# Optimization experiments

Hardware: AMD Instinct MI355X
Metric: run time of the kernel (lower is better)

## Reference

```python
import jax, jax.numpy as jnp
import numpy as np

G = 16  # self.group
K = 3   # unfold/fold kernel size


def setup_inputs() -> dict:
    key = jax.random.key(0)
    feature = jax.random.normal(key, (2, 128, 192, 192), dtype=jnp.float32)
    return {"feature": feature}


def reference(feature):
    B, C, H, W = feature.shape
    Cg = C // G
    Hm, Wm = H - K + 1, W - K + 1
    L = Hm * Wm

    # --- nn.Unfold(kernel_size=3), all groups at once ---
    # patches[b, c, k, y, x] with k = ki*3 + kj (channel-major flat = c*9 + k)
    slices = [feature[:, :, ki:ki + Hm, kj:kj + Wm] for ki in range(K) for kj in range(K)]
    patches = jnp.stack(slices, axis=2)                 # [B, C, 9, Hm, Wm]
    # per-group series flat dim is Cg*9 (order cg*9+k); chunk(9) -> reshape [9, Cg]
    motif = patches.reshape(B, G, Cg * 9, L).reshape(B, G, 9, Cg, L)  # [B,G,9,Cg,L]

    # --- cdist + diag=inf + argmin (squared distances: same argmin as p=2) ---
    gram = jnp.einsum('bgjcl,bgjdl->bgjcd', motif, motif)   # [B,G,9,Cg,Cg]
    sq = jnp.einsum('bgjcl,bgjcl->bgjc', motif, motif)      # [B,G,9,Cg]
    d2 = sq[..., :, None] + sq[..., None, :] - 2.0 * gram
    eye = jnp.eye(Cg, dtype=bool)
    d2 = jnp.where(eye, jnp.inf, d2)
    nn_idx = jnp.argmin(d2, axis=-1)                        # [B,G,9,Cg] int

    # --- torch.unique loop overwrites motif_new: only the LAST (max) unique
    # index and its count survive ---
    u_max = jnp.max(nn_idx, axis=-1)                        # [B,G,9]
    c_max = jnp.sum(nn_idx == u_max[..., None], axis=-1).astype(feature.dtype)  # [B,G,9]

    motif_nn = jnp.take_along_axis(motif, u_max[..., None, None], axis=3)  # [B,G,9,1,L]
    # float '//' in torch is floor division
    term = jnp.floor(motif * motif_nn * c_max[..., None, None] / Cg)
    # l == 0 branch drops the '+ motif' term
    batch_mask = (jnp.arange(B) != 0).astype(feature.dtype).reshape(B, 1, 1, 1, 1)
    out_ser = motif * batch_mask + term                     # [B,G,9,Cg,L]

    # --- nn.Fold: input layout reinterpreted as (channel, kernel) flat = c*9+k ---
    ser2 = out_ser.reshape(B, G, 9 * Cg, L).reshape(B, G, Cg, 9, Hm, Wm)
    out = jnp.zeros((B, G, Cg, H, W), feature.dtype)
    for k in range(K * K):
        ki, kj = k // K, k % K
        out = out.at[:, :, :, ki:ki + Hm, kj:kj + Wm].add(ser2[:, :, :, k])
    return out.reshape(B, C, H, W)
```

## Files before the change

### kernel.cpp

```cpp
#include <hip/hip_runtime.h>
#include <hip/hip_bf16.h>
#include <math.h>

#define BB 2
#define CC 128
#define GG 16
#define CG 8
#define HH 192
#define WW 192
#define HM 190
#define WM 190
#define LL (HM * WM)
#define HWSZ (HH * WW)
#define NTRIPLE (BB * GG * 9)
#define SPLIT 6
#define ROWS_PER_SLICE 32

typedef float float4a __attribute__((ext_vector_type(4), aligned(4)));
typedef float float4v __attribute__((ext_vector_type(4)));

__device__ float g_part[NTRIPLE * SPLIT * 36];
__device__ int g_rel[BB * GG * 72];
__device__ float g_scl[BB * GG * 72];

constexpr bool row_used(int J, int ci, int ki) {
  for (int d = 0; d < 8; ++d) {
    const int f = 8 * J + d;
    if ((f / 9 - (8 * J) / 9) == ci && (f % 9) / 3 == ki) return true;
  }
  return false;
}

template <int J>
__device__ __forceinline__ void gram_slice(const float* __restrict__ pA,
                                           const float* __restrict__ pB,
                                           int y0, int rows, int tid,
                                           float acc[36]) {
  constexpr int CA = (8 * J) / 9;
  constexpr int CB = (8 * J + 7) / 9;
  constexpr int NCH = (CB > CA) ? 2 : 1;

  const int ngrp = rows * 47;
  for (int q = tid; q < ngrp; q += 128) {
    const int y = y0 + q / 47;
    const int x0 = (q % 47) * 4;
    const int ro = y * WW + x0;

    float w[NCH][3][8];
#pragma unroll
    for (int ci = 0; ci < NCH; ++ci) {
      const float* pc = ci ? pB : pA;
#pragma unroll
      for (int ki = 0; ki < 3; ++ki) {
        if (row_used(J, ci, ki)) {
          const float4v a = *(const float4v*)(pc + ro + ki * WW);
          const float4v bq = *(const float4v*)(pc + ro + ki * WW + 4);
          w[ci][ki][0] = a.x; w[ci][ki][1] = a.y;
          w[ci][ki][2] = a.z; w[ci][ki][3] = a.w;
          w[ci][ki][4] = bq.x; w[ci][ki][5] = bq.y;
          w[ci][ki][6] = bq.z; w[ci][ki][7] = bq.w;
        }
      }
    }
#pragma unroll
    for (int d = 0; d < 8; ++d) {
      constexpr_helper_sq:;
      const int f = 8 * J + d;
      const int ci = f / 9 - CA;
      const int k = f % 9;
      const int ki = k / 3, kj = k % 3;
      float s = 0.0f;
#pragma unroll
      for (int e = 0; e < 4; ++e) s += w[ci][ki][kj + e] * w[ci][ki][kj + e];
      acc[d] += s;
    }
    int p = 8;
#pragma unroll
    for (int c = 0; c < 8; ++c) {
      const int f1 = 8 * J + c;
      const int ci1 = f1 / 9 - CA;
      const int k1 = f1 % 9;
      const int ki1 = k1 / 3, kj1 = k1 % 3;
#pragma unroll
      for (int d = c + 1; d < 8; ++d) {
        const int f2 = 8 * J + d;
        const int ci2 = f2 / 9 - CA;
        const int k2 = f2 % 9;
        const int ki2 = k2 / 3, kj2 = k2 % 3;
        float s = 0.0f;
#pragma unroll
        for (int e = 0; e < 4; ++e)
          s += w[ci1][ki1][kj1 + e] * w[ci2][ki2][kj2 + e];
        acc[p++] += s;
      }
    }
  }

  const int ncl = rows * 2;
  for (int t = tid; t < ncl; t += 128) {
    const int y = y0 + t / 2;
    const int x = 188 + (t & 1);
    float v[8];
#pragma unroll
    for (int d = 0; d < 8; ++d) {
      const int f = 8 * J + d;
      const int ci = f / 9 - CA;
      const int k = f % 9;
      const int ki = k / 3, kj = k % 3;
      v[d] = (ci ? pB : pA)[(y + ki) * WW + x + kj];
    }
#pragma unroll
    for (int d = 0; d < 8; ++d) acc[d] += v[d] * v[d];
    int p = 8;
#pragma unroll
    for (int c = 0; c < 8; ++c)
#pragma unroll
      for (int d = c + 1; d < 8; ++d) acc[p++] += v[c] * v[d];
  }
}

__global__ __launch_bounds__(128, 2) void phase1a_kernel(
    const float* __restrict__ feat) {
  const int B = blockIdx.x;
  const int xcd = B & 7;
  const int slot = B >> 3;
  const int unit = xcd * 4 + slot / 54;
  const int r = slot % 54;
  const int j = r / 6;
  const int sl = r % 6;
  const int b = unit >> 4;
  const int g = unit & 15;

  const int cA = (8 * j) / 9;
  const int cB = (8 * j + 7) / 9;
  const float* pA = feat + (size_t)(b * CC + g * CG + cA) * HWSZ;
  const float* pB = feat + (size_t)(b * CC + g * CG + cB) * HWSZ;

  const int y0 = sl * ROWS_PER_SLICE;
  const int y1 = (y0 + ROWS_PER_SLICE < HM) ? y0 + ROWS_PER_SLICE : HM;
  const int rows = y1 - y0;
  const int tid = (int)threadIdx.x;

  float acc[36];
#pragma unroll
  for (int i = 0; i < 36; ++i) acc[i] = 0.0f;

  switch (j) {
    case 0: gram_slice<0>(pA, pB, y0, rows, tid, acc); break;
    case 1: gram_slice<1>(pA, pB, y0, rows, tid, acc); break;
    case 2: gram_slice<2>(pA, pB, y0, rows, tid, acc); break;
    case 3: gram_slice<3>(pA, pB, y0, rows, tid, acc); break;
    case 4: gram_slice<4>(pA, pB, y0, rows, tid, acc); break;
    case 5: gram_slice<5>(pA, pB, y0, rows, tid, acc); break;
    case 6: gram_slice<6>(pA, pB, y0, rows, tid, acc); break;
    case 7: gram_slice<7>(pA, pB, y0, rows, tid, acc); break;
    default: gram_slice<8>(pA, pB, y0, rows, tid, acc); break;
  }

  __shared__ float red[36 * 2];
  const int lane = tid & 63;
  const int wave = tid >> 6;
#pragma unroll
  for (int i = 0; i < 36; ++i) {
    float v = acc[i];
    for (int o = 32; o > 0; o >>= 1) v += __shfl_down(v, o, 64);
    if (lane == 0) red[i * 2 + wave] = v;
  }
  __syncthreads();
  if (tid < 36) {
    const int i = tid;
    const int tri = unit * 9 + j;
    g_part[(tri * SPLIT + sl) * 36 + i] = red[i * 2] + red[i * 2 + 1];
  }
}

__global__ __launch_bounds__(64) void phase1b_kernel() {
  const int tri = blockIdx.x * 64 + (int)threadIdx.x;
  if (tri >= NTRIPLE) return;
  const int b = tri / (GG * 9);
  const int rem = tri % (GG * 9);
  const int g = rem / 9;
  const int j = rem % 9;

  float tot[36];
#pragma unroll
  for (int i = 0; i < 36; ++i) tot[i] = 0.0f;
  for (int s = 0; s < SPLIT; ++s)
#pragma unroll
    for (int i = 0; i < 36; ++i) tot[i] += g_part[(tri * SPLIT + s) * 36 + i];

  float sq[8], gm[8][8];
#pragma unroll
  for (int i = 0; i < 8; ++i) sq[i] = tot[i];
  {
    int p = 8;
    for (int c = 0; c < 8; ++c)
      for (int d = c + 1; d < 8; ++d) {
        gm[c][d] = tot[p];
        gm[d][c] = tot[p];
        ++p;
      }
  }
  int nn[8];
  for (int c = 0; c < 8; ++c) {
    float best = INFINITY;
    int bi = 0;
    for (int d = 0; d < 8; ++d) {
      if (d == c) continue;
      const float d2 = sq[c] + sq[d] - 2.0f * gm[c][d];
      if (d2 < best) {
        best = d2;
        bi = d;
      }
    }
    nn[c] = bi;
  }
  int um = 0;
  for (int c = 0; c < 8; ++c) um = um > nn[c] ? um : nn[c];
  int cnt = 0;
  for (int c = 0; c < 8; ++c) cnt += (nn[c] == um) ? 1 : 0;

  const float sc = (float)cnt * 0.125f;
  const int fn = j * 8 + um;
  const int cn = fn / 9;
  const int kn = fn % 9;
  const int kin = kn / 3, kjn = kn % 3;
  for (int d = 0; d < 8; ++d) {
    const int f = j * 8 + d;
    const int cl = f / 9;
    const int k = f % 9;
    const int ki = k / 3, kj = k % 3;
    const int rel = (cn - cl) * HWSZ + (kin - ki) * WW + (kjn - kj);
    const int tix = (b * GG + g) * 72 + f;
    g_rel[tix] = rel;
    g_scl[tix] = sc;
  }
}

__global__ __launch_bounds__(256) void phase2_main_kernel(
    const float* __restrict__ feat, float* __restrict__ out) {
  const int B = blockIdx.x;
  const int xcd = B & 7;
  const int slot = B >> 3;
  const int unit = xcd * 4 + slot / 144;
  const int r = slot % 144;
  const int cl = r / 18;
  const int blk = r % 18;
  const int plane = unit * 8 + cl;

  const int tbase = unit * 72 + cl * 9;
  int rel[9];
  float scl[9];
#pragma unroll
  for (int k = 0; k < 9; ++k) {
    rel[k] = g_rel[tbase + k];
    scl[k] = g_scl[tbase + k];
  }

  const float* pb = feat + (size_t)plane * HWSZ;
  float* ob = out + (size_t)plane * HWSZ;
  const bool b1 = (unit >= GG);
  const int i0 = blk * 2048 + (int)threadIdx.x * 4;

#pragma unroll
  for (int gidx = 0; gidx < 2; ++gidx) {
    const int inner = i0 + gidx * 1024;
    const int h = inner / WW;
    const int w0 = inner % WW;
    if (h >= 2 && h < HM && w0 >= 4 && w0 < 188) {
      const float* p = pb + inner;
      const float4v v = *(const float4v*)p;
      float4v acc = {0.0f, 0.0f, 0.0f, 0.0f};
#pragma unroll
      for (int k = 0; k < 9; ++k) {
        const float4a n = *(const float4a*)(p + rel[k]);
        const float s = scl[k];
        acc.x += floorf(v.x * n.x * s);
        acc.y += floorf(v.y * n.y * s);
        acc.z += floorf(v.z * n.z * s);
        acc.w += floorf(v.w * n.w * s);
      }
      if (b1) {
        acc.x += 9.0f * v.x;
        acc.y += 9.0f * v.y;
        acc.z += 9.0f * v.z;
        acc.w += 9.0f * v.w;
      }
      *(float4v*)(ob + inner) = acc;
    }
  }
}

__global__ __launch_bounds__(256) void phase2_edge_kernel(
    const float* __restrict__ feat, float* __restrict__ out) {
  const int gid = blockIdx.x * 256 + (int)threadIdx.x;
  const int plane = gid / 2272;
  const int ei = gid % 2272;
  int h, w;
  if (ei < 768) {
    const int r = ei / WW;
    h = (r < 2) ? r : r + 188;
    w = ei % WW;
  } else {
    const int e2 = ei - 768;
    h = 2 + (e2 >> 3);
    const int w8 = e2 & 7;
    w = (w8 < 4) ? w8 : w8 + 184;
  }
  const int g = (plane % CC) >> 3;
  const int cl = (plane % CC) & 7;
  const int tbase = ((plane / CC) * GG + g) * 72 + cl * 9;

  int rel[9];
  float scl[9];
#pragma unroll
  for (int k = 0; k < 9; ++k) {
    rel[k] = g_rel[tbase + k];
    scl[k] = g_scl[tbase + k];
  }

  const int idx = plane * HWSZ + h * WW + w;
  const float* p = feat + idx;
  const float v = *p;
  float acc = 0.0f;
  int nv = 0;
#pragma unroll
  for (int k = 0; k < 9; ++k) {
    const int ki = k / 3, kj = k % 3;
    const int y = h - ki, x = w - kj;
    const bool valid = ((unsigned)y < (unsigned)HM) & ((unsigned)x < (unsigned)WM);
    const int o = valid ? rel[k] : 0;
    const float n = p[o];
    const float fl = floorf(v * n * scl[k]);
    acc += valid ? fl : 0.0f;
    nv += valid ? 1 : 0;
  }
  if (plane >= CC) acc += (float)nv * v;
  out[idx] = acc;
}

extern "C" void kernel_launch(void* const* d_in, const int* in_sizes, int n_in,
                              void* d_out, int out_size, void* d_ws,
                              size_t ws_size, hipStream_t stream) {
  const float* feat = (const float*)d_in[0];
  float* out = (float*)d_out;
  (void)d_ws;
  (void)ws_size;

  phase1a_kernel<<<NTRIPLE * SPLIT, 128, 0, stream>>>(feat);
  phase1b_kernel<<<(NTRIPLE + 63) / 64, 64, 0, stream>>>();

  phase2_main_kernel<<<BB * CC * 18, 256, 0, stream>>>(feat, out);
  phase2_edge_kernel<<<2272, 256, 0, stream>>>(feat, out);
}
```

Baseline: 131.7 us.

## Fuse partial-gram reduction into phase1 and edge handling into phase2 main kernel

The separate phase1b reduction kernel is removed. The last-arriving block for each triple, found with an atomic counter and threadfences, now sums the split partials, computes the nearest-neighbour index and scale, and resets the counter. The separate edge kernel is also folded into the main phase2 kernel as a scalar fallback branch for border pixels. This removes two kernel launches and their inter-kernel gaps, at the cost of atomics, fences and some divergence in the edge blocks.

```diff
diff --git a/kernel.cpp b/kernel.cpp
--- a/kernel.cpp
+++ b/kernel.cpp
@@ -1,5 +1,4 @@
 #include <hip/hip_runtime.h>
-#include <hip/hip_bf16.h>
 #include <math.h>
 
 #define BB 2
@@ -22,6 +21,7 @@
 __device__ float g_part[NTRIPLE * SPLIT * 36];
 __device__ int g_rel[BB * GG * 72];
 __device__ float g_scl[BB * GG * 72];
+__device__ int g_cnt[NTRIPLE];
 
 constexpr bool row_used(int J, int ci, int ki) {
   for (int d = 0; d < 8; ++d) {
@@ -64,7 +64,6 @@
     }
 #pragma unroll
     for (int d = 0; d < 8; ++d) {
-      constexpr_helper_sq:;
       const int f = 8 * J + d;
       const int ci = f / 9 - CA;
       const int k = f % 9;
@@ -119,7 +118,7 @@
   }
 }
 
-__global__ __launch_bounds__(128, 2) void phase1a_kernel(
+__global__ __launch_bounds__(128, 2) void phase1_kernel(
     const float* __restrict__ feat) {
   const int B = blockIdx.x;
   const int xcd = B & 7;
@@ -167,77 +166,84 @@
     if (lane == 0) red[i * 2 + wave] = v;
   }
   __syncthreads();
+  const int tri = unit * 9 + j;
   if (tid < 36) {
-    const int i = tid;
-    const int tri = unit * 9 + j;
-    g_part[(tri * SPLIT + sl) * 36 + i] = red[i * 2] + red[i * 2 + 1];
-  }
-}
-
-__global__ __launch_bounds__(64) void phase1b_kernel() {
-  const int tri = blockIdx.x * 64 + (int)threadIdx.x;
-  if (tri >= NTRIPLE) return;
-  const int b = tri / (GG * 9);
-  const int rem = tri % (GG * 9);
-  const int g = rem / 9;
-  const int j = rem % 9;
-
-  float tot[36];
-#pragma unroll
-  for (int i = 0; i < 36; ++i) tot[i] = 0.0f;
-  for (int s = 0; s < SPLIT; ++s)
-#pragma unroll
-    for (int i = 0; i < 36; ++i) tot[i] += g_part[(tri * SPLIT + s) * 36 + i];
-
-  float sq[8], gm[8][8];
-#pragma unroll
-  for (int i = 0; i < 8; ++i) sq[i] = tot[i];
-  {
-    int p = 8;
-    for (int c = 0; c < 8; ++c)
-      for (int d = c + 1; d < 8; ++d) {
-        gm[c][d] = tot[p];
-        gm[d][c] = tot[p];
-        ++p;
-      }
-  }
-  int nn[8];
-  for (int c = 0; c < 8; ++c) {
-    float best = INFINITY;
-    int bi = 0;
-    for (int d = 0; d < 8; ++d) {
-      if (d == c) continue;
-      const float d2 = sq[c] + sq[d] - 2.0f * gm[c][d];
-      if (d2 < best) {
-        best = d2;
-        bi = d;
-      }
-    }
-    nn[c] = bi;
-  }
-  int um = 0;
-  for (int c = 0; c < 8; ++c) um = um > nn[c] ? um : nn[c];
-  int cnt = 0;
-  for (int c = 0; c < 8; ++c) cnt += (nn[c] == um) ? 1 : 0;
-
-  const float sc = (float)cnt * 0.125f;
-  const int fn = j * 8 + um;
-  const int cn = fn / 9;
-  const int kn = fn % 9;
-  const int kin = kn / 3, kjn = kn % 3;
-  for (int d = 0; d < 8; ++d) {
-    const int f = j * 8 + d;
+    g_part[(tri * SPLIT + sl) * 36 + tid] = red[tid * 2] + red[tid * 2 + 1];
+  }
+
+  __threadfence();
+  __shared__ int s_last;
+  if (tid == 0) s_last = (atomicAdd(&g_cnt[tri], 1) == SPLIT - 1) ? 1 : 0;
+  __syncthreads();
+  if (!s_last) return;
+  __threadfence();
+
+  __shared__ float s_tot[36];
+  if (tid < 36) {
+    float t = 0.0f;
+    for (int s = 0; s < SPLIT; ++s)
+      t += g_part[(tri * SPLIT + s) * 36 + tid];
+    s_tot[tid] = t;
+  }
+  __syncthreads();
+
+  __shared__ int s_um;
+  __shared__ float s_sc;
+  if (tid == 0) {
+    float sq[8], gm[8][8];
+#pragma unroll
+    for (int i = 0; i < 8; ++i) sq[i] = s_tot[i];
+    {
+      int p = 8;
+      for (int c = 0; c < 8; ++c)
+        for (int d = c + 1; d < 8; ++d) {
+          gm[c][d] = s_tot[p];
+          gm[d][c] = s_tot[p];
+          ++p;
+        }
+    }
+    int nn[8];
+    for (int c = 0; c < 8; ++c) {
+      float best = INFINITY;
+      int bi = 0;
+      for (int d = 0; d < 8; ++d) {
+        if (d == c) continue;
+        const float d2 = sq[c] + sq[d] - 2.0f * gm[c][d];
+        if (d2 < best) {
+          best = d2;
+          bi = d;
+        }
+      }
+      nn[c] = bi;
+    }
+    int um = 0;
+    for (int c = 0; c < 8; ++c) um = um > nn[c] ? um : nn[c];
+    int cnt = 0;
+    for (int c = 0; c < 8; ++c) cnt += (nn[c] == um) ? 1 : 0;
+    s_um = um;
+    s_sc = (float)cnt * 0.125f;
+    g_cnt[tri] = 0;
+  }
+  __syncthreads();
+
+  if (tid < 8) {
+    const int um = s_um;
+    const int fn = j * 8 + um;
+    const int cn = fn / 9;
+    const int kn = fn % 9;
+    const int kin = kn / 3, kjn = kn % 3;
+    const int f = j * 8 + tid;
     const int cl = f / 9;
     const int k = f % 9;
     const int ki = k / 3, kj = k % 3;
     const int rel = (cn - cl) * HWSZ + (kin - ki) * WW + (kjn - kj);
-    const int tix = (b * GG + g) * 72 + f;
+    const int tix = unit * 72 + f;
     g_rel[tix] = rel;
-    g_scl[tix] = sc;
-  }
-}
-
-__global__ __launch_bounds__(256) void phase2_main_kernel(
+    g_scl[tix] = s_sc;
+  }
+}
+
+__global__ __launch_bounds__(256) void phase2_kernel(
     const float* __restrict__ feat, float* __restrict__ out) {
   const int B = blockIdx.x;
   const int xcd = B & 7;
@@ -287,56 +293,31 @@
         acc.w += 9.0f * v.w;
       }
       *(float4v*)(ob + inner) = acc;
-    }
-  }
-}
-
-__global__ __launch_bounds__(256) void phase2_edge_kernel(
-    const float* __restrict__ feat, float* __restrict__ out) {
-  const int gid = blockIdx.x * 256 + (int)threadIdx.x;
-  const int plane = gid / 2272;
-  const int ei = gid % 2272;
-  int h, w;
-  if (ei < 768) {
-    const int r = ei / WW;
-    h = (r < 2) ? r : r + 188;
-    w = ei % WW;
-  } else {
-    const int e2 = ei - 768;
-    h = 2 + (e2 >> 3);
-    const int w8 = e2 & 7;
-    w = (w8 < 4) ? w8 : w8 + 184;
-  }
-  const int g = (plane % CC) >> 3;
-  const int cl = (plane % CC) & 7;
-  const int tbase = ((plane / CC) * GG + g) * 72 + cl * 9;
-
-  int rel[9];
-  float scl[9];
-#pragma unroll
-  for (int k = 0; k < 9; ++k) {
-    rel[k] = g_rel[tbase + k];
-    scl[k] = g_scl[tbase + k];
-  }
-
-  const int idx = plane * HWSZ + h * WW + w;
-  const float* p = feat + idx;
-  const float v = *p;
-  float acc = 0.0f;
-  int nv = 0;
-#pragma unroll
-  for (int k = 0; k < 9; ++k) {
-    const int ki = k / 3, kj = k % 3;
-    const int y = h - ki, x = w - kj;
-    const bool valid = ((unsigned)y < (unsigned)HM) & ((unsigned)x < (unsigned)WM);
-    const int o = valid ? rel[k] : 0;
-    const float n = p[o];
-    const float fl = floorf(v * n * scl[k]);
-    acc += valid ? fl : 0.0f;
-    nv += valid ? 1 : 0;
-  }
-  if (plane >= CC) acc += (float)nv * v;
-  out[idx] = acc;
+    } else {
+#pragma unroll
+      for (int e = 0; e < 4; ++e) {
+        const int w = w0 + e;
+        const float* p = pb + inner + e;
+        const float v = *p;
+        float acc = 0.0f;
+        int nv = 0;
+#pragma unroll
+        for (int k = 0; k < 9; ++k) {
+          const int ki = k / 3, kj = k % 3;
+          const int y = h - ki, x = w - kj;
+          const bool valid =
+              ((unsigned)y < (unsigned)HM) & ((unsigned)x < (unsigned)WM);
+          const int o = valid ? rel[k] : 0;
+          const float n = p[o];
+          const float fl = floorf(v * n * scl[k]);
+          acc += valid ? fl : 0.0f;
+          nv += valid ? 1 : 0;
+        }
+        if (b1) acc += (float)nv * v;
+        ob[inner + e] = acc;
+      }
+    }
+  }
 }
 
 extern "C" void kernel_launch(void* const* d_in, const int* in_sizes, int n_in,
@@ -346,10 +327,10 @@
   float* out = (float*)d_out;
   (void)d_ws;
   (void)ws_size;
-
-  phase1a_kernel<<<NTRIPLE * SPLIT, 128, 0, stream>>>(feat);
-  phase1b_kernel<<<(NTRIPLE + 63) / 64, 64, 0, stream>>>();
-
-  phase2_main_kernel<<<BB * CC * 18, 256, 0, stream>>>(feat, out);
-  phase2_edge_kernel<<<2272, 256, 0, stream>>>(feat, out);
-}
+  (void)in_sizes;
+  (void)n_in;
+  (void)out_size;
+
+  phase1_kernel<<<NTRIPLE * SPLIT, 128, 0, stream>>>(feat);
+  phase2_kernel<<<BB * CC * 18, 256, 0, stream>>>(feat, out);
+}
```

Result: slower. 206.1 us (+56.4%).

## Fuse edge handling into main phase2 kernel and widen phase1 blocks

Applied to the files above, without the earlier changes.

Phase1 now runs 256 threads per block instead of 128, and its cross-wave reduction covers four waves. The two phase2 kernels become one: each block covers a quarter plane over nine iterations, and border pixels go through an inline scalar path instead of a separate edge kernel. This removes one kernel launch and adds parallelism in the Gram pass, at the cost of higher register pressure and some divergence in the border branches.

```diff
diff --git a/kernel.cpp b/kernel.cpp
--- a/kernel.cpp
+++ b/kernel.cpp
@@ -1,5 +1,4 @@
 #include <hip/hip_runtime.h>
-#include <hip/hip_bf16.h>
 #include <math.h>
 
 #define BB 2
@@ -10,7 +9,6 @@
 #define WW 192
 #define HM 190
 #define WM 190
-#define LL (HM * WM)
 #define HWSZ (HH * WW)
 #define NTRIPLE (BB * GG * 9)
 #define SPLIT 6
@@ -41,7 +39,7 @@
   constexpr int NCH = (CB > CA) ? 2 : 1;
 
   const int ngrp = rows * 47;
-  for (int q = tid; q < ngrp; q += 128) {
+  for (int q = tid; q < ngrp; q += 256) {
     const int y = y0 + q / 47;
     const int x0 = (q % 47) * 4;
     const int ro = y * WW + x0;
@@ -64,7 +62,6 @@
     }
 #pragma unroll
     for (int d = 0; d < 8; ++d) {
-      constexpr_helper_sq:;
       const int f = 8 * J + d;
       const int ci = f / 9 - CA;
       const int k = f % 9;
@@ -97,7 +94,7 @@
   }
 
   const int ncl = rows * 2;
-  for (int t = tid; t < ncl; t += 128) {
+  for (int t = tid; t < ncl; t += 256) {
     const int y = y0 + t / 2;
     const int x = 188 + (t & 1);
     float v[8];
@@ -119,7 +116,7 @@
   }
 }
 
-__global__ __launch_bounds__(128, 2) void phase1a_kernel(
+__global__ __launch_bounds__(256, 4) void phase1_kernel(
     const float* __restrict__ feat) {
   const int B = blockIdx.x;
   const int xcd = B & 7;
@@ -157,20 +154,21 @@
     default: gram_slice<8>(pA, pB, y0, rows, tid, acc); break;
   }
 
-  __shared__ float red[36 * 2];
+  __shared__ float red[36 * 4];
   const int lane = tid & 63;
   const int wave = tid >> 6;
 #pragma unroll
   for (int i = 0; i < 36; ++i) {
     float v = acc[i];
     for (int o = 32; o > 0; o >>= 1) v += __shfl_down(v, o, 64);
-    if (lane == 0) red[i * 2 + wave] = v;
+    if (lane == 0) red[i * 4 + wave] = v;
   }
   __syncthreads();
   if (tid < 36) {
-    const int i = tid;
     const int tri = unit * 9 + j;
-    g_part[(tri * SPLIT + sl) * 36 + i] = red[i * 2] + red[i * 2 + 1];
+    g_part[(tri * SPLIT + sl) * 36 + tid] =
+        ((red[tid * 4] + red[tid * 4 + 1]) + red[tid * 4 + 2]) +
+        red[tid * 4 + 3];
   }
 }
 
@@ -237,16 +235,17 @@
   }
 }
 
-__global__ __launch_bounds__(256) void phase2_main_kernel(
+__global__ __launch_bounds__(256) void phase2_kernel(
     const float* __restrict__ feat, float* __restrict__ out) {
   const int B = blockIdx.x;
   const int xcd = B & 7;
   const int slot = B >> 3;
-  const int unit = xcd * 4 + slot / 144;
-  const int r = slot % 144;
-  const int cl = r / 18;
-  const int blk = r % 18;
+  const int unit = xcd * 4 + slot / 32;
+  const int r = slot % 32;
+  const int cl = r / 4;
+  const int qblk = r % 4;
   const int plane = unit * 8 + cl;
+  const int tid = (int)threadIdx.x;
 
   const int tbase = unit * 72 + cl * 9;
   int rel[9];
@@ -260,10 +259,9 @@
   const float* pb = feat + (size_t)plane * HWSZ;
   float* ob = out + (size_t)plane * HWSZ;
   const bool b1 = (unit >= GG);
-  const int i0 = blk * 2048 + (int)threadIdx.x * 4;
-
-#pragma unroll
-  for (int gidx = 0; gidx < 2; ++gidx) {
+  const int i0 = qblk * 9216 + tid * 4;
+
+  for (int gidx = 0; gidx < 9; ++gidx) {
     const int inner = i0 + gidx * 1024;
     const int h = inner / WW;
     const int w0 = inner % WW;
@@ -287,56 +285,31 @@
         acc.w += 9.0f * v.w;
       }
       *(float4v*)(ob + inner) = acc;
-    }
-  }
-}
-
-__global__ __launch_bounds__(256) void phase2_edge_kernel(
-    const float* __restrict__ feat, float* __restrict__ out) {
-  const int gid = blockIdx.x * 256 + (int)threadIdx.x;
-  const int plane = gid / 2272;
-  const int ei = gid % 2272;
-  int h, w;
-  if (ei < 768) {
-    const int r = ei / WW;
-    h = (r < 2) ? r : r + 188;
-    w = ei % WW;
-  } else {
-    const int e2 = ei - 768;
-    h = 2 + (e2 >> 3);
-    const int w8 = e2 & 7;
-    w = (w8 < 4) ? w8 : w8 + 184;
-  }
-  const int g = (plane % CC) >> 3;
-  const int cl = (plane % CC) & 7;
-  const int tbase = ((plane / CC) * GG + g) * 72 + cl * 9;
-
-  int rel[9];
-  float scl[9];
-#pragma unroll
-  for (int k = 0; k < 9; ++k) {
-    rel[k] = g_rel[tbase + k];
-    scl[k] = g_scl[tbase + k];
-  }
-
-  const int idx = plane * HWSZ + h * WW + w;
-  const float* p = feat + idx;
-  const float v = *p;
-  float acc = 0.0f;
-  int nv = 0;
-#pragma unroll
-  for (int k = 0; k < 9; ++k) {
-    const int ki = k / 3, kj = k % 3;
-    const int y = h - ki, x = w - kj;
-    const bool valid = ((unsigned)y < (unsigned)HM) & ((unsigned)x < (unsigned)WM);
-    const int o = valid ? rel[k] : 0;
-    const float n = p[o];
-    const float fl = floorf(v * n * scl[k]);
-    acc += valid ? fl : 0.0f;
-    nv += valid ? 1 : 0;
-  }
-  if (plane >= CC) acc += (float)nv * v;
-  out[idx] = acc;
+    } else {
+#pragma unroll
+      for (int e = 0; e < 4; ++e) {
+        const int w = w0 + e;
+        const float* p = pb + inner + e;
+        const float v = *p;
+        float acc = 0.0f;
+        int nv = 0;
+#pragma unroll
+        for (int k = 0; k < 9; ++k) {
+          const int ki = k / 3, kj = k % 3;
+          const int y = h - ki, x = w - kj;
+          const bool valid =
+              ((unsigned)y < (unsigned)HM) & ((unsigned)x < (unsigned)WM);
+          const int o = valid ? rel[k] : 0;
+          const float n = p[o];
+          const float fl = floorf(v * n * scl[k]);
+          acc += valid ? fl : 0.0f;
+          nv += valid ? 1 : 0;
+        }
+        if (b1) acc += (float)nv * v;
+        ob[inner + e] = acc;
+      }
+    }
+  }
 }
 
 extern "C" void kernel_launch(void* const* d_in, const int* in_sizes, int n_in,
@@ -346,10 +319,11 @@
   float* out = (float*)d_out;
   (void)d_ws;
   (void)ws_size;
-
-  phase1a_kernel<<<NTRIPLE * SPLIT, 128, 0, stream>>>(feat);
+  (void)in_sizes;
+  (void)n_in;
+  (void)out_size;
+
+  phase1_kernel<<<NTRIPLE * SPLIT, 256, 0, stream>>>(feat);
   phase1b_kernel<<<(NTRIPLE + 63) / 64, 64, 0, stream>>>();
-
-  phase2_main_kernel<<<BB * CC * 18, 256, 0, stream>>>(feat, out);
-  phase2_edge_kernel<<<2272, 256, 0, stream>>>(feat, out);
-}
+  phase2_kernel<<<BB * CC * 4, 256, 0, stream>>>(feat, out);
+}
```

Result: slower. 149.3 us (+13.3%).

## Stage gram-slice input rows in shared memory and parallelize per-triple reduction

Applied to the files above, without the earlier changes.

The phase-1 Gram kernel now copies each region's one or two channel rows (plus a 2-row halo) into LDS with coalesced float4 loads. The windowed dot products then read from LDS instead of issuing overlapping global loads. The row split moves from 6 slices of 32 rows to 8 regions of 24 rows, blocks grow to 256 threads, and the finalize kernel uses one block per triple so 36 threads sum the partials in parallel. This costs about 40 KB of LDS per block, which may limit occupancy, plus extra halo-row loads.

```diff
diff --git a/kernel.cpp b/kernel.cpp
--- a/kernel.cpp
+++ b/kernel.cpp
@@ -1,5 +1,4 @@
 #include <hip/hip_runtime.h>
-#include <hip/hip_bf16.h>
 #include <math.h>
 
 #define BB 2
@@ -10,11 +9,10 @@
 #define WW 192
 #define HM 190
 #define WM 190
-#define LL (HM * WM)
 #define HWSZ (HH * WW)
 #define NTRIPLE (BB * GG * 9)
-#define SPLIT 6
-#define ROWS_PER_SLICE 32
+#define SPLIT 8
+#define RREG 24
 
 typedef float float4a __attribute__((ext_vector_type(4), aligned(4)));
 typedef float float4v __attribute__((ext_vector_type(4)));
@@ -32,29 +30,26 @@
 }
 
 template <int J>
-__device__ __forceinline__ void gram_slice(const float* __restrict__ pA,
-                                           const float* __restrict__ pB,
-                                           int y0, int rows, int tid,
-                                           float acc[36]) {
+__device__ __forceinline__ void gram_region(float* s_ch, int rows, int tid,
+                                            float acc[36]) {
   constexpr int CA = (8 * J) / 9;
   constexpr int CB = (8 * J + 7) / 9;
   constexpr int NCH = (CB > CA) ? 2 : 1;
 
   const int ngrp = rows * 47;
-  for (int q = tid; q < ngrp; q += 128) {
-    const int y = y0 + q / 47;
+  for (int q = tid; q < ngrp; q += 256) {
+    const int ly = q / 47;
     const int x0 = (q % 47) * 4;
-    const int ro = y * WW + x0;
 
     float w[NCH][3][8];
 #pragma unroll
     for (int ci = 0; ci < NCH; ++ci) {
-      const float* pc = ci ? pB : pA;
 #pragma unroll
       for (int ki = 0; ki < 3; ++ki) {
         if (row_used(J, ci, ki)) {
-          const float4v a = *(const float4v*)(pc + ro + ki * WW);
-          const float4v bq = *(const float4v*)(pc + ro + ki * WW + 4);
+          const float* rp = s_ch + (ci * 26 + ly + ki) * 192 + x0;
+          const float4v a = *(const float4v*)rp;
+          const float4v bq = *(const float4v*)(rp + 4);
           w[ci][ki][0] = a.x; w[ci][ki][1] = a.y;
           w[ci][ki][2] = a.z; w[ci][ki][3] = a.w;
           w[ci][ki][4] = bq.x; w[ci][ki][5] = bq.y;
@@ -64,7 +59,6 @@
     }
 #pragma unroll
     for (int d = 0; d < 8; ++d) {
-      constexpr_helper_sq:;
       const int f = 8 * J + d;
       const int ci = f / 9 - CA;
       const int k = f % 9;
@@ -97,8 +91,8 @@
   }
 
   const int ncl = rows * 2;
-  for (int t = tid; t < ncl; t += 128) {
-    const int y = y0 + t / 2;
+  for (int t = tid; t < ncl; t += 256) {
+    const int ly = t / 2;
     const int x = 188 + (t & 1);
     float v[8];
 #pragma unroll
@@ -107,7 +101,7 @@
       const int ci = f / 9 - CA;
       const int k = f % 9;
       const int ki = k / 3, kj = k % 3;
-      v[d] = (ci ? pB : pA)[(y + ki) * WW + x + kj];
+      v[d] = s_ch[(ci * 26 + ly + ki) * 192 + x + kj];
     }
 #pragma unroll
     for (int d = 0; d < 8; ++d) acc[d] += v[d] * v[d];
@@ -119,85 +113,105 @@
   }
 }
 
-__global__ __launch_bounds__(128, 2) void phase1a_kernel(
+__global__ __launch_bounds__(256, 2) void phase1_kernel(
     const float* __restrict__ feat) {
   const int B = blockIdx.x;
   const int xcd = B & 7;
   const int slot = B >> 3;
-  const int unit = xcd * 4 + slot / 54;
-  const int r = slot % 54;
-  const int j = r / 6;
-  const int sl = r % 6;
+  const int unit = xcd * 4 + slot / 72;
+  const int rem = slot % 72;
+  const int j = rem / 8;
+  const int region = rem % 8;
   const int b = unit >> 4;
   const int g = unit & 15;
 
   const int cA = (8 * j) / 9;
   const int cB = (8 * j + 7) / 9;
+  const int nch = (cB > cA) ? 2 : 1;
   const float* pA = feat + (size_t)(b * CC + g * CG + cA) * HWSZ;
   const float* pB = feat + (size_t)(b * CC + g * CG + cB) * HWSZ;
 
-  const int y0 = sl * ROWS_PER_SLICE;
-  const int y1 = (y0 + ROWS_PER_SLICE < HM) ? y0 + ROWS_PER_SLICE : HM;
-  const int rows = y1 - y0;
+  const int y0 = region * RREG;
+  const int rows = (y0 + RREG <= HM) ? RREG : HM - y0;
   const int tid = (int)threadIdx.x;
 
+  __shared__ float s_ch[2 * 26 * 192];
+
+  const int rs = rows + 2;
+  const int nst = nch * rs * 48;
+  for (int t = tid; t < nst; t += 256) {
+    const int ch = t / (rs * 48);
+    const int r2 = t % (rs * 48);
+    const int row = r2 / 48;
+    const int quad = r2 % 48;
+    const float4v val =
+        *(const float4v*)((ch ? pB : pA) + (y0 + row) * WW + quad * 4);
+    *(float4v*)(s_ch + (ch * 26 + row) * 192 + quad * 4) = val;
+  }
+  __syncthreads();
+
   float acc[36];
 #pragma unroll
   for (int i = 0; i < 36; ++i) acc[i] = 0.0f;
 
   switch (j) {
-    case 0: gram_slice<0>(pA, pB, y0, rows, tid, acc); break;
-    case 1: gram_slice<1>(pA, pB, y0, rows, tid, acc); break;
-    case 2: gram_slice<2>(pA, pB, y0, rows, tid, acc); break;
-    case 3: gram_slice<3>(pA, pB, y0, rows, tid, acc); break;
-    case 4: gram_slice<4>(pA, pB, y0, rows, tid, acc); break;
-    case 5: gram_slice<5>(pA, pB, y0, rows, tid, acc); break;
-    case 6: gram_slice<6>(pA, pB, y0, rows, tid, acc); break;
-    case 7: gram_slice<7>(pA, pB, y0, rows, tid, acc); break;
-    default: gram_slice<8>(pA, pB, y0, rows, tid, acc); break;
-  }
-
-  __shared__ float red[36 * 2];
+    case 0: gram_region<0>(s_ch, rows, tid, acc); break;
+    case 1: gram_region<1>(s_ch, rows, tid, acc); break;
+    case 2: gram_region<2>(s_ch, rows, tid, acc); break;
+    case 3: gram_region<3>(s_ch, rows, tid, acc); break;
+    case 4: gram_region<4>(s_ch, rows, tid, acc); break;
+    case 5: gram_region<5>(s_ch, rows, tid, acc); break;
+    case 6: gram_region<6>(s_ch, rows, tid, acc); break;
+    case 7: gram_region<7>(s_ch, rows, tid, acc); break;
+    default: gram_region<8>(s_ch, rows, tid, acc); break;
+  }
+
+  __syncthreads();
+  float* red = s_ch;
   const int lane = tid & 63;
   const int wave = tid >> 6;
 #pragma unroll
   for (int i = 0; i < 36; ++i) {
     float v = acc[i];
     for (int o = 32; o > 0; o >>= 1) v += __shfl_down(v, o, 64);
-    if (lane == 0) red[i * 2 + wave] = v;
+    if (lane == 0) red[i * 4 + wave] = v;
   }
   __syncthreads();
   if (tid < 36) {
-    const int i = tid;
     const int tri = unit * 9 + j;
-    g_part[(tri * SPLIT + sl) * 36 + i] = red[i * 2] + red[i * 2 + 1];
+    g_part[(tri * SPLIT + region) * 36 + tid] =
+        ((red[tid * 4] + red[tid * 4 + 1]) + red[tid * 4 + 2]) +
+        red[tid * 4 + 3];
   }
 }
 
 __global__ __launch_bounds__(64) void phase1b_kernel() {
-  const int tri = blockIdx.x * 64 + (int)threadIdx.x;
-  if (tri >= NTRIPLE) return;
+  const int tri = blockIdx.x;
+  const int tid = (int)threadIdx.x;
   const int b = tri / (GG * 9);
   const int rem = tri % (GG * 9);
   const int g = rem / 9;
   const int j = rem % 9;
 
-  float tot[36];
-#pragma unroll
-  for (int i = 0; i < 36; ++i) tot[i] = 0.0f;
-  for (int s = 0; s < SPLIT; ++s)
-#pragma unroll
-    for (int i = 0; i < 36; ++i) tot[i] += g_part[(tri * SPLIT + s) * 36 + i];
+  __shared__ float s_tot[36];
+  if (tid < 36) {
+    float t = 0.0f;
+    for (int s = 0; s < SPLIT; ++s)
+      t += g_part[(tri * SPLIT + s) * 36 + tid];
+    s_tot[tid] = t;
+  }
+  __syncthreads();
+  if (tid != 0) return;
 
   float sq[8], gm[8][8];
 #pragma unroll
-  for (int i = 0; i < 8; ++i) sq[i] = tot[i];
+  for (int i = 0; i < 8; ++i) sq[i] = s_tot[i];
   {
     int p = 8;
     for (int c = 0; c < 8; ++c)
       for (int d = c + 1; d < 8; ++d) {
-        gm[c][d] = tot[p];
-        gm[d][c] = tot[p];
+        gm[c][d] = s_tot[p];
+        gm[d][c] = s_tot[p];
         ++p;
       }
   }
@@ -346,10 +360,12 @@
   float* out = (float*)d_out;
   (void)d_ws;
   (void)ws_size;
-
-  phase1a_kernel<<<NTRIPLE * SPLIT, 128, 0, stream>>>(feat);
-  phase1b_kernel<<<(NTRIPLE + 63) / 64, 64, 0, stream>>>();
-
+  (void)in_sizes;
+  (void)n_in;
+  (void)out_size;
+
+  phase1_kernel<<<NTRIPLE * SPLIT, 256, 0, stream>>>(feat);
+  phase1b_kernel<<<NTRIPLE, 64, 0, stream>>>();
   phase2_main_kernel<<<BB * CC * 18, 256, 0, stream>>>(feat, out);
   phase2_edge_kernel<<<2272, 256, 0, stream>>>(feat, out);
 }
```

Result: slower. 143.8 us (+9.1%).
